# Kernel tuning notes

Hardware: AMD Instinct MI355X
Metric: run time of the kernel (lower is better)

## Reference

```python
import jax, jax.numpy as jnp
import numpy as np

WS = 32          # window_size; N = WS*WS tokens
NH = 8           # num_heads
HD = 64          # head_dim
DIM = 512        # model dim (= NH*HD)
B = 16
N = WS * WS


def _rel_index() -> np.ndarray:
    """Relative position index, identical to the torch __init__ construction."""
    coords = np.stack(np.meshgrid(np.arange(WS), np.arange(WS), indexing='ij'))
    coords = coords.reshape(2, -1)                       # [2, N]
    rel = coords[:, :, None] - coords[:, None, :]        # [2, N, N]
    rel = rel.transpose(1, 2, 0).copy()                  # [N, N, 2]
    rel[..., 0] += WS - 1
    rel[..., 1] += WS - 1
    rel[..., 0] *= 2 * WS - 1
    return rel.sum(-1).astype(np.int32)                  # [N, N], values in [0, (2WS-1)^2)


def setup_inputs() -> dict:
    key = jax.random.key(0)
    ks = jax.random.split(key, 5)
    s = DIM ** -0.5
    return {
        "x": jax.random.normal(ks[0], (B, N, DIM), jnp.float32),
        "qkv_w": jax.random.normal(ks[1], (3 * NH * HD, DIM), jnp.float32) * s,
        "qkv_b": jnp.zeros((3 * NH * HD,), jnp.float32),
        "proj_w": jax.random.normal(ks[2], (DIM, NH * HD), jnp.float32) * s,
        "proj_b": jnp.zeros((DIM,), jnp.float32),
        "bias_table": jax.random.normal(ks[3], ((2 * WS - 1) ** 2, NH), jnp.float32) * 0.02,
        "rel_index": jnp.asarray(_rel_index()),
    }


def reference(x, qkv_w, qkv_b, proj_w, proj_b, bias_table, rel_index):
    Bb, Nn, C = x.shape
    qkv = (x @ qkv_w.T + qkv_b).reshape(Bb, Nn, 3, NH, HD)
    q, k, v = jnp.moveaxis(qkv, 2, 0)                    # each [B, N, NH, HD]
    q = q * (HD ** -0.5)
    attn = jnp.einsum('bnhd,bmhd->bhnm', q, k)           # [B, NH, N, N]
    bias = bias_table[rel_index]                         # gather -> [N, N, NH]
    attn = attn + jnp.transpose(bias, (2, 0, 1))[None]
    attn = jax.nn.softmax(attn, axis=-1)                 # dropout p=0 (eval)
    out = jnp.einsum('bhnm,bmhd->bnhd', attn, v).reshape(Bb, Nn, NH * HD)
    out = out @ proj_w.T + proj_b                        # [B, N, DIM]
    return jnp.transpose(out, (0, 2, 1)).reshape(Bb, DIM, WS, WS)
```

## Files before the change

### kernel.cpp

```cpp
#include <hip/hip_runtime.h>
#include <hip/hip_bf16.h>


typedef __attribute__((ext_vector_type(4))) float  f32x4;
typedef __attribute__((ext_vector_type(8))) short  s16x8;
typedef __attribute__((ext_vector_type(4))) short  s16x4;

#define LOG2E 1.44269504f

__device__ __forceinline__ short f2bf(float f) {
    union { float f; unsigned u; } v; v.f = f;
    unsigned r = v.u + 0x7fffu + ((v.u >> 16) & 1u);
    return (short)(r >> 16);
}
__device__ __forceinline__ float u2f(unsigned u) {
    union { unsigned u; float f; } v; v.u = u; return v.f;
}
__device__ __forceinline__ unsigned f2u(float f) {
    union { float f; unsigned u; } v; v.f = f; return v.u;
}
__device__ __forceinline__ unsigned pack2(float a, float b) {
    unsigned ua = f2u(a), ub = f2u(b);
    ua += 0x7fffu + ((ua >> 16) & 1u);
    ub += 0x7fffu + ((ub >> 16) & 1u);
    return __builtin_amdgcn_perm(ub, ua, 0x07060302);
}
__device__ __forceinline__ s16x8 ld_frag(const short* p) {
    s16x4 lo = *(const s16x4*)p;
    s16x4 hi = *(const s16x4*)(p + 4);
    s16x8 v;
    v[0]=lo[0]; v[1]=lo[1]; v[2]=lo[2]; v[3]=lo[3];
    v[4]=hi[0]; v[5]=hi[1]; v[6]=hi[2]; v[7]=hi[3];
    return v;
}
__device__ __forceinline__ void st8(short* p, s16x8 v) {
    s16x4 lo, hi;
    lo[0]=v[0]; lo[1]=v[1]; lo[2]=v[2]; lo[3]=v[3];
    hi[0]=v[4]; hi[1]=v[5]; hi[2]=v[6]; hi[3]=v[7];
    *(s16x4*)p = lo;
    *(s16x4*)(p + 4) = hi;
}

__global__ void cvt_kernel(const float* __restrict__ src, short* __restrict__ dst) {
    int i = blockIdx.x * 256 + threadIdx.x;
    f32x4 v = ((const f32x4*)src)[i];
    s16x4 o;
    o[0]=f2bf(v[0]); o[1]=f2bf(v[1]); o[2]=f2bf(v[2]); o[3]=f2bf(v[3]);
    ((s16x4*)dst)[i] = o;
}

__global__ void bias_expand(const float* __restrict__ table, const int* __restrict__ ridx,
                            short* __restrict__ out) {
    int i = blockIdx.x * 256 + threadIdx.x;
    int n = i >> 10, m = i & 1023;
    int idx = ridx[i];
    const float* t = table + idx * 8;
    int pos = ((n*8 + (m >> 7))*4 + ((m >> 2) & 3))*32 + ((m >> 4) & 7)*4 + (m & 3);
    #pragma unroll
    for (int h = 0; h < 8; h++)
        out[h * 1048576 + pos] = f2bf(t[h] * LOG2E);
}

__global__ __launch_bounds__(256) void qkv_gemm(
    const short* __restrict__ Xb, const short* __restrict__ W,
    const float* __restrict__ bias,
    short* __restrict__ qb, short* __restrict__ kb, short* __restrict__ vtb)
{
    __shared__ short As[128][36];
    __shared__ short Bs[128][36];
    const int tid = threadIdx.x;
    const int lane = tid & 63, w = tid >> 6;
    const int quad = lane >> 4, l16 = lane & 15;
    const int m0 = blockIdx.y * 128, n0 = blockIdx.x * 128;
    const int wm = (w >> 1) * 64, wn = (w & 1) * 64;
    f32x4 acc[4][4] = {};

    const int sr = tid >> 2;
    const int sc = (tid & 3) * 8;

    for (int k0 = 0; k0 < 512; k0 += 32) {
        __syncthreads();
        #pragma unroll
        for (int p = 0; p < 2; p++) {
            int r = sr + p * 64;
            st8(&As[r][sc], *(const s16x8*)(Xb + (m0 + r) * 512 + k0 + sc));
            st8(&Bs[r][sc], *(const s16x8*)(W  + (n0 + r) * 512 + k0 + sc));
        }
        __syncthreads();
        s16x8 af[4], bfr[4];
        #pragma unroll
        for (int i = 0; i < 4; i++) af[i]  = ld_frag(&As[wm + i*16 + l16][quad*8]);
        #pragma unroll
        for (int j = 0; j < 4; j++) bfr[j] = ld_frag(&Bs[wn + j*16 + l16][quad*8]);
        #pragma unroll
        for (int i = 0; i < 4; i++)
            #pragma unroll
            for (int j = 0; j < 4; j++)
                acc[i][j] = __builtin_amdgcn_mfma_f32_16x16x32_bf16(af[i], bfr[j], acc[i][j], 0, 0, 0);
    }

    #pragma unroll
    for (int j = 0; j < 4; j++) {
        int col = n0 + wn + j*16 + l16;
        int which = col >> 9, rem = col & 511, h = rem >> 6, d = rem & 63;
        float bv = bias[col];
        #pragma unroll
        for (int i = 0; i < 4; i++) {
            int row = m0 + wm + i*16 + quad*4;
            int bi = row >> 10, n = row & 1023;
            if (which == 2) {
                float v0 = acc[i][j][0] + bv, v1 = acc[i][j][1] + bv;
                float v2 = acc[i][j][2] + bv, v3 = acc[i][j][3] + bv;
                uint2 pk; pk.x = pack2(v0, v1); pk.y = pack2(v2, v3);
                *(uint2*)&vtb[((bi*8 + h)*64 + d)*1024 + n] = pk;
            } else {
                #pragma unroll
                for (int r = 0; r < 4; r++) {
                    float v = acc[i][j][r] + bv;
                    if (which == 0)
                        qb[((bi*8 + h)*1024 + n + r)*64 + d] = f2bf(v * (0.125f * LOG2E));
                    else
                        kb[((bi*8 + h)*1024 + n + r)*64 + d] = f2bf(v);
                }
            }
        }
    }
}

__global__ __launch_bounds__(512, 4) void attn_kernel(
    const short* __restrict__ qbuf, const short* __restrict__ kbuf,
    const short* __restrict__ vtbuf, const short* __restrict__ bxp,
    short* __restrict__ ao)
{
    __shared__ __align__(16) short smem[25344];
    short* R1 = smem;
    short* Vs = smem + 16896;

    const int bh = blockIdx.y;
    const int b = bh >> 3, h = bh & 7;
    const int q0 = blockIdx.x * 128;
    const int tid = threadIdx.x, lane = tid & 63, w = tid >> 6;
    const int quad = lane >> 4, l16 = lane & 15;

    const short* qg = qbuf + (bh*1024 + q0) * 64;
    const short* kg = kbuf + bh * 65536;
    const short* vg = vtbuf + bh * 65536;

    {
        int r = tid >> 3, c = (tid & 7) * 8;
        #pragma unroll
        for (int p = 0; p < 2; p++)
            st8(&R1[(r + p*64)*68 + c], *(const s16x8*)(qg + (r + p*64)*64 + c));
    }
    __syncthreads();
    s16x8 aq[2];
    aq[0] = ld_frag(&R1[(w*16 + l16)*68 + quad*8]);
    aq[1] = ld_frag(&R1[(w*16 + l16)*68 + 32 + quad*8]);

    float mrow = -1e30f, lrow = 0.f;
    f32x4 oacc[4] = {};
    short* Pw = R1 + w * 2112;
    const short* bbase = bxp + h*1048576 + ((q0 + w*16 + l16)*8)*128 + quad*32;

    for (int it = 0; it < 8; it++) {
        const int k0 = it * 128;
        __syncthreads();

        uint4 bw[4];
        {
            const uint4* bp = (const uint4*)(bbase + it*128);
            #pragma unroll
            for (int j = 0; j < 4; j++) bw[j] = bp[j];
        }

        {
            int r = tid >> 3, c = (tid & 7) * 8;
            #pragma unroll
            for (int p = 0; p < 2; p++)
                st8(&R1[(r + p*64)*68 + c], *(const s16x8*)(kg + (k0 + r + p*64)*64 + c));
        }
        {
            int r = tid >> 4, c = (tid & 15) * 8;
            #pragma unroll
            for (int p = 0; p < 2; p++)
                st8(&Vs[(r + p*32)*132 + c], *(const s16x8*)(vg + (r + p*32)*1024 + k0 + c));
        }
        __syncthreads();

        f32x4 s[8];
        #pragma unroll
        for (int nf = 0; nf < 8; nf++) {
            unsigned ua = (nf & 1) ? bw[nf >> 1].z : bw[nf >> 1].x;
            unsigned ub = (nf & 1) ? bw[nf >> 1].w : bw[nf >> 1].y;
            s[nf][0] = u2f(ua << 16); s[nf][1] = u2f(ua & 0xffff0000u);
            s[nf][2] = u2f(ub << 16); s[nf][3] = u2f(ub & 0xffff0000u);
            s16x8 bk0 = ld_frag(&R1[(nf*16 + l16)*68 + quad*8]);
            s16x8 bk1 = ld_frag(&R1[(nf*16 + l16)*68 + 32 + quad*8]);
            s[nf] = __builtin_amdgcn_mfma_f32_16x16x32_bf16(bk0, aq[0], s[nf], 0, 0, 0);
            s[nf] = __builtin_amdgcn_mfma_f32_16x16x32_bf16(bk1, aq[1], s[nf], 0, 0, 0);
        }

        float mx = s[0][0];
        #pragma unroll
        for (int nf = 0; nf < 8; nf++) {
            float a = fmaxf(s[nf][0], s[nf][1]), c = fmaxf(s[nf][2], s[nf][3]);
            mx = fmaxf(mx, fmaxf(a, c));
        }
        mx = fmaxf(mx, __shfl_xor(mx, 16));
        mx = fmaxf(mx, __shfl_xor(mx, 32));
        float mnew = fmaxf(mrow, mx);
        float alpha = __builtin_exp2f(mrow - mnew);
        mrow = mnew;
        float rs = 0.f;
        #pragma unroll
        for (int nf = 0; nf < 8; nf++)
            #pragma unroll
            for (int r = 0; r < 4; r++) {
                float p = __builtin_exp2f(s[nf][r] - mnew);
                s[nf][r] = p;
                rs += p;
            }
        rs += __shfl_xor(rs, 16);
        rs += __shfl_xor(rs, 32);
        lrow = lrow * alpha + rs;

        float a_r[4];
        #pragma unroll
        for (int r = 0; r < 4; r++) a_r[r] = __shfl(alpha, quad*4 + r);
        #pragma unroll
        for (int df = 0; df < 4; df++)
            #pragma unroll
            for (int r = 0; r < 4; r++)
                oacc[df][r] *= a_r[r];

        __syncthreads();

        #pragma unroll
        for (int nf = 0; nf < 8; nf++) {
            uint2 pk;
            pk.x = pack2(s[nf][0], s[nf][1]);
            pk.y = pack2(s[nf][2], s[nf][3]);
            *(uint2*)&Pw[l16*132 + nf*16 + quad*4] = pk;
        }
        asm volatile("s_waitcnt lgkmcnt(0)" ::: "memory");

        #pragma unroll
        for (int ks = 0; ks < 4; ks++) {
            s16x8 ap = ld_frag(&Pw[l16*132 + ks*32 + quad*8]);
            #pragma unroll
            for (int df = 0; df < 4; df++) {
                s16x8 bv = ld_frag(&Vs[(df*16 + l16)*132 + ks*32 + quad*8]);
                oacc[df] = __builtin_amdgcn_mfma_f32_16x16x32_bf16(ap, bv, oacc[df], 0, 0, 0);
            }
        }
    }

    float inv_r[4];
    #pragma unroll
    for (int r = 0; r < 4; r++) inv_r[r] = 1.0f / __shfl(lrow, quad*4 + r);
    #pragma unroll
    for (int r = 0; r < 4; r++) {
        int n = q0 + w*16 + quad*4 + r;
        #pragma unroll
        for (int df = 0; df < 4; df++)
            ao[(b*1024 + n)*512 + h*64 + df*16 + l16] = f2bf(oacc[df][r] * inv_r[r]);
    }
}

__global__ __launch_bounds__(256) void proj_gemm(
    const short* __restrict__ A, const short* __restrict__ W,
    const float* __restrict__ bias, float* __restrict__ out)
{
    __shared__ __align__(16) short smemp[2*128*36];
    short (*As)[36] = (short(*)[36])smemp;
    short (*Bs)[36] = (short(*)[36])(smemp + 128*36);
    const int tid = threadIdx.x;
    const int lane = tid & 63, w = tid >> 6;
    const int quad = lane >> 4, l16 = lane & 15;
    const int m0 = blockIdx.y * 128, n0 = blockIdx.x * 128;
    const int wm = (w >> 1) * 64, wn = (w & 1) * 64;
    f32x4 acc[4][4] = {};

    const int sr = tid >> 2;
    const int sc = (tid & 3) * 8;

    for (int k0 = 0; k0 < 512; k0 += 32) {
        __syncthreads();
        #pragma unroll
        for (int p = 0; p < 2; p++) {
            int r = sr + p * 64;
            st8(&As[r][sc], *(const s16x8*)(A + (m0 + r) * 512 + k0 + sc));
            st8(&Bs[r][sc], *(const s16x8*)(W + (n0 + r) * 512 + k0 + sc));
        }
        __syncthreads();
        s16x8 af[4], bfr[4];
        #pragma unroll
        for (int i = 0; i < 4; i++) af[i]  = ld_frag(&As[wm + i*16 + l16][quad*8]);
        #pragma unroll
        for (int j = 0; j < 4; j++) bfr[j] = ld_frag(&Bs[wn + j*16 + l16][quad*8]);
        #pragma unroll
        for (int i = 0; i < 4; i++)
            #pragma unroll
            for (int j = 0; j < 4; j++)
                acc[i][j] = __builtin_amdgcn_mfma_f32_16x16x32_bf16(af[i], bfr[j], acc[i][j], 0, 0, 0);
    }

    const int bi = m0 >> 10, nbase = m0 & 1023;
    float* Ts = (float*)smemp;
    #pragma unroll
    for (int ci = 0; ci < 4; ci++) {
        __syncthreads();
        if ((w & 1) == (ci >> 1)) {
            #pragma unroll
            for (int jj = 0; jj < 2; jj++) {
                int j = (ci & 1) * 2 + jj;
                int c = n0 + wn + j*16 + l16;
                float bv = bias[c];
                int cl = jj*16 + l16;
                #pragma unroll
                for (int i = 0; i < 4; i++) {
                    f32x4 v = acc[i][j];
                    v[0] += bv; v[1] += bv; v[2] += bv; v[3] += bv;
                    *(f32x4*)&Ts[cl*132 + wm + i*16 + quad*4] = v;
                }
            }
        }
        __syncthreads();
        #pragma unroll
        for (int p = 0; p < 4; p++) {
            int row = (tid >> 5) + p*8, col = (tid & 31)*4;
            f32x4 v = *(const f32x4*)&Ts[row*132 + col];
            *(f32x4*)&out[(bi*512 + n0 + ci*32 + row)*1024 + nbase + col] = v;
        }
    }
}

extern "C" void kernel_launch(void* const* d_in, const int* in_sizes, int n_in,
                              void* d_out, int out_size, void* d_ws, size_t ws_size,
                              hipStream_t stream) {
    const float* x      = (const float*)d_in[0];
    const float* qkv_w  = (const float*)d_in[1];
    const float* qkv_b  = (const float*)d_in[2];
    const float* proj_w = (const float*)d_in[3];
    const float* proj_b = (const float*)d_in[4];
    const float* btab   = (const float*)d_in[5];
    const int*   ridx   = (const int*)d_in[6];
    float* out = (float*)d_out;

    short* ws    = (short*)d_ws;
    short* wqkv  = ws;
    short* wproj = wqkv + 1536*512;
    short* qb    = wproj + 512*512;
    short* kb    = qb  + 16*8*1024*64;
    short* vtb   = kb  + 16*8*1024*64;
    short* bx    = vtb + 16*8*1024*64;
    short* ao    = bx  + 8*1024*1024;
    short* xb    = ao;

    cvt_kernel<<<8192, 256, 0, stream>>>(x, xb);
    cvt_kernel<<<768, 256, 0, stream>>>(qkv_w, wqkv);
    cvt_kernel<<<256, 256, 0, stream>>>(proj_w, wproj);
    bias_expand<<<4096, 256, 0, stream>>>(btab, ridx, bx);
    qkv_gemm<<<dim3(12, 128), 256, 0, stream>>>(xb, wqkv, qkv_b, qb, kb, vtb);
    attn_kernel<<<dim3(8, 128), 512, 0, stream>>>(qb, kb, vtb, bx, ao);
    proj_gemm<<<dim3(4, 128), 256, 0, stream>>>(ao, wproj, proj_b, out);
}
```

Before: 263.5 us.

## Lazy softmax rescaling, hardware bf16 pack, deferred row-sum reduce, MFMA priority hints

The online softmax now rescales the running max and output accumulator only when some lane's new max exceeds the stored max by more than 8 (log2 units), skipping the shuffle-based max reduction and the accumulator multiply in most iterations. The per-row sum is kept per lane and reduced across lanes once after the loop. Software bf16 rounding is replaced by the v_cvt_pk_bf16_f32 instruction, and s_setprio raises wave priority around the MFMA blocks. This trades a bounded growth of unnormalized exponentials for less per-tile work, and relies on fp32 headroom staying safe.

```diff
diff --git a/kernel.cpp b/kernel.cpp
--- a/kernel.cpp
+++ b/kernel.cpp
@@ -16,14 +16,10 @@
 __device__ __forceinline__ float u2f(unsigned u) {
     union { unsigned u; float f; } v; v.u = u; return v.f;
 }
-__device__ __forceinline__ unsigned f2u(float f) {
-    union { float f; unsigned u; } v; v.f = f; return v.u;
-}
-__device__ __forceinline__ unsigned pack2(float a, float b) {
-    unsigned ua = f2u(a), ub = f2u(b);
-    ua += 0x7fffu + ((ua >> 16) & 1u);
-    ub += 0x7fffu + ((ub >> 16) & 1u);
-    return __builtin_amdgcn_perm(ub, ua, 0x07060302);
+__device__ __forceinline__ unsigned cvtpk(float lo, float hi) {
+    unsigned r;
+    asm("v_cvt_pk_bf16_f32 %0, %1, %2" : "=v"(r) : "v"(lo), "v"(hi));
+    return r;
 }
 __device__ __forceinline__ s16x8 ld_frag(const short* p) {
     s16x4 lo = *(const s16x4*)p;
@@ -111,7 +107,7 @@
             if (which == 2) {
                 float v0 = acc[i][j][0] + bv, v1 = acc[i][j][1] + bv;
                 float v2 = acc[i][j][2] + bv, v3 = acc[i][j][3] + bv;
-                uint2 pk; pk.x = pack2(v0, v1); pk.y = pack2(v2, v3);
+                uint2 pk; pk.x = cvtpk(v0, v1); pk.y = cvtpk(v2, v3);
                 *(uint2*)&vtb[((bi*8 + h)*64 + d)*1024 + n] = pk;
             } else {
                 #pragma unroll
@@ -188,6 +184,7 @@
         __syncthreads();
 
         f32x4 s[8];
+        __builtin_amdgcn_s_setprio(1);
         #pragma unroll
         for (int nf = 0; nf < 8; nf++) {
             unsigned ua = (nf & 1) ? bw[nf >> 1].z : bw[nf >> 1].x;
@@ -199,6 +196,7 @@
             s[nf] = __builtin_amdgcn_mfma_f32_16x16x32_bf16(bk0, aq[0], s[nf], 0, 0, 0);
             s[nf] = __builtin_amdgcn_mfma_f32_16x16x32_bf16(bk1, aq[1], s[nf], 0, 0, 0);
         }
+        __builtin_amdgcn_s_setprio(0);
 
         float mx = s[0][0];
         #pragma unroll
@@ -206,44 +204,45 @@
             float a = fmaxf(s[nf][0], s[nf][1]), c = fmaxf(s[nf][2], s[nf][3]);
             mx = fmaxf(mx, fmaxf(a, c));
         }
-        mx = fmaxf(mx, __shfl_xor(mx, 16));
-        mx = fmaxf(mx, __shfl_xor(mx, 32));
-        float mnew = fmaxf(mrow, mx);
-        float alpha = __builtin_exp2f(mrow - mnew);
-        mrow = mnew;
+        if (!__all(mx - mrow <= 8.0f)) {
+            float mr = fmaxf(mx, __shfl_xor(mx, 16));
+            mr = fmaxf(mr, __shfl_xor(mr, 32));
+            float mnew = fmaxf(mrow, mr);
+            float alpha = __builtin_exp2f(mrow - mnew);
+            mrow = mnew;
+            lrow *= alpha;
+            float a_r[4];
+            #pragma unroll
+            for (int r = 0; r < 4; r++) a_r[r] = __shfl(alpha, quad*4 + r);
+            #pragma unroll
+            for (int df = 0; df < 4; df++)
+                #pragma unroll
+                for (int r = 0; r < 4; r++)
+                    oacc[df][r] *= a_r[r];
+        }
         float rs = 0.f;
         #pragma unroll
         for (int nf = 0; nf < 8; nf++)
             #pragma unroll
             for (int r = 0; r < 4; r++) {
-                float p = __builtin_exp2f(s[nf][r] - mnew);
+                float p = __builtin_exp2f(s[nf][r] - mrow);
                 s[nf][r] = p;
                 rs += p;
             }
-        rs += __shfl_xor(rs, 16);
-        rs += __shfl_xor(rs, 32);
-        lrow = lrow * alpha + rs;
-
-        float a_r[4];
-        #pragma unroll
-        for (int r = 0; r < 4; r++) a_r[r] = __shfl(alpha, quad*4 + r);
-        #pragma unroll
-        for (int df = 0; df < 4; df++)
-            #pragma unroll
-            for (int r = 0; r < 4; r++)
-                oacc[df][r] *= a_r[r];
+        lrow += rs;
 
         __syncthreads();
 
         #pragma unroll
         for (int nf = 0; nf < 8; nf++) {
             uint2 pk;
-            pk.x = pack2(s[nf][0], s[nf][1]);
-            pk.y = pack2(s[nf][2], s[nf][3]);
+            pk.x = cvtpk(s[nf][0], s[nf][1]);
+            pk.y = cvtpk(s[nf][2], s[nf][3]);
             *(uint2*)&Pw[l16*132 + nf*16 + quad*4] = pk;
         }
         asm volatile("s_waitcnt lgkmcnt(0)" ::: "memory");
 
+        __builtin_amdgcn_s_setprio(1);
         #pragma unroll
         for (int ks = 0; ks < 4; ks++) {
             s16x8 ap = ld_frag(&Pw[l16*132 + ks*32 + quad*8]);
@@ -253,8 +252,11 @@
                 oacc[df] = __builtin_amdgcn_mfma_f32_16x16x32_bf16(ap, bv, oacc[df], 0, 0, 0);
             }
         }
-    }
-
+        __builtin_amdgcn_s_setprio(0);
+    }
+
+    lrow += __shfl_xor(lrow, 16);
+    lrow += __shfl_xor(lrow, 32);
     float inv_r[4];
     #pragma unroll
     for (int r = 0; r < 4; r++) inv_r[r] = 1.0f / __shfl(lrow, quad*4 + r);
```

Measured after the change: 256.4 us. -2.7%, faster.
